# Kernel optimization log

Measured on AMD Instinct MI355X. Metric: run time of the kernel, lower is better.

The kernel has to match this reference:

```python
import jax, jax.numpy as jnp
import numpy as np

B, V, C, D, H, W = 2, 2, 32, 48, 128, 160


def _conv2d(x, w, pad):
    return jax.lax.conv_general_dilated(x, w, (1, 1), [(pad, pad), (pad, pad)],
                                        dimension_numbers=('NCHW', 'OIHW', 'NCHW'))


def _bilinear_sample(fea, px, py):
    # fea: [b,c,h,w]; px,py: [b,N] pixel coords (grid_sample bilinear, zeros padding, align_corners=True)
    b, c, h, w = fea.shape
    fea_flat = fea.reshape(b, c, h * w)
    x0 = jnp.floor(px); y0 = jnp.floor(py)
    wx = px - x0; wy = py - y0
    x0i = x0.astype(jnp.int32); y0i = y0.astype(jnp.int32)

    def corner(xi, yi, wgt):
        valid = (xi >= 0) & (xi < w) & (yi >= 0) & (yi < h)
        idx = jnp.clip(yi, 0, h - 1) * w + jnp.clip(xi, 0, w - 1)
        g = jax.vmap(lambda f, i: f[:, i])(fea_flat, idx)  # [b,c,N]
        return g * (wgt * valid)[:, None, :]

    return (corner(x0i, y0i, (1 - wx) * (1 - wy))
            + corner(x0i + 1, y0i, wx * (1 - wy))
            + corner(x0i, y0i + 1, (1 - wx) * wy)
            + corner(x0i + 1, y0i + 1, wx * wy))


def _homo_warp(src_fea, src_proj, ref_proj, depth_values):
    # classic MVSNet 3D homography warp -> [b,c,d,h,w]
    b, c, h, w = src_fea.shape
    d = depth_values.shape[1]
    proj = src_proj @ jnp.linalg.inv(ref_proj)
    rot, trans = proj[:, :3, :3], proj[:, :3, 3]
    yy, xx = jnp.meshgrid(jnp.arange(h, dtype=src_fea.dtype), jnp.arange(w, dtype=src_fea.dtype), indexing='ij')
    xyz = jnp.stack([xx.ravel(), yy.ravel(), jnp.ones(h * w, src_fea.dtype)])  # [3,hw]
    rot_xyz = jnp.einsum('bij,jn->bin', rot, xyz)  # [b,3,hw]
    pxyz = rot_xyz[:, :, None, :] * depth_values.reshape(b, 1, d, h * w) + trans[:, :, None, None]
    z = pxyz[:, 2]
    z = jnp.where(jnp.abs(z) < 1e-6, 1e-6, z)
    px = (pxyz[:, 0] / z).reshape(b, d * h * w)
    py = (pxyz[:, 1] / z).reshape(b, d * h * w)
    return _bilinear_sample(src_fea, px, py).reshape(b, c, d, h, w)


def setup_inputs() -> dict:
    key = jax.random.key(0)
    ks = jax.random.split(key, 8)
    ref_fea = jax.random.normal(ks[0], (B, C, H, W), jnp.float32)
    src_feas = jax.random.normal(ks[1], (V, B, C, H, W), jnp.float32)
    ref_nc = jax.random.uniform(ks[2], (B, 1, H, W), jnp.float32)
    ref_nc_sum = jax.random.uniform(ks[3], (B, 1, H, W), jnp.float32)
    src_nc_sums = jax.random.uniform(ks[4], (V, B, 1, H, W), jnp.float32)
    # structured projections: slot 0 = extrinsic 4x4, slot 1 holds K in [:3,:3]
    K = np.eye(4, dtype=np.float32)
    K[0, 0] = K[1, 1] = 200.0; K[0, 2] = W / 2.0; K[1, 2] = H / 2.0
    projs = np.zeros((B, V + 1, 2, 4, 4), np.float32)
    for v in range(V + 1):
        E = np.eye(4, dtype=np.float32)
        if v > 0:
            E[0, 3] = 2.0 * v  # horizontal baseline
        projs[:, v, 0] = E
        projs[:, v, 1] = K
    proj_matrices = jnp.asarray(projs)
    dvals = jnp.linspace(425.0, 900.0, D, dtype=jnp.float32)
    depth_values = jnp.broadcast_to(dvals[None, :, None, None], (B, D, H, W))
    vis_w1 = jax.random.normal(ks[5], (32, 2, 3, 3), jnp.float32) * 0.1
    vis_bn_gamma = jnp.ones((32,), jnp.float32)
    vis_bn_beta = jnp.zeros((32,), jnp.float32)
    vis_w2 = jax.random.normal(ks[6], (1, 32, 1, 1), jnp.float32) * 0.1
    vis_b2 = jnp.zeros((1,), jnp.float32)
    reg_w = jax.random.normal(ks[7], (C,), jnp.float32) * 0.1
    reg_b = jnp.zeros((1,), jnp.float32)
    return dict(ref_fea=ref_fea, src_feas=src_feas, ref_nc=ref_nc, ref_nc_sum=ref_nc_sum,
                src_nc_sums=src_nc_sums, proj_matrices=proj_matrices, depth_values=depth_values,
                vis_w1=vis_w1, vis_bn_gamma=vis_bn_gamma, vis_bn_beta=vis_bn_beta,
                vis_w2=vis_w2, vis_b2=vis_b2, reg_w=reg_w, reg_b=reg_b)


def reference(ref_fea, src_feas, ref_nc, ref_nc_sum, src_nc_sums, proj_matrices,
              depth_values, vis_w1, vis_bn_gamma, vis_bn_beta, vis_w2, vis_b2, reg_w, reg_b):
    b, c, h, w = ref_fea.shape
    d = depth_values.shape[1]
    v_src = src_feas.shape[0]
    rp = proj_matrices[:, 0]
    ref_proj_new = rp[:, 0].at[:, :3, :4].set(rp[:, 1, :3, :3] @ rp[:, 0, :3, :4])
    bn_scale = vis_bn_gamma / jnp.sqrt(jnp.float32(1.0) + 1e-5)  # eval BN: running mean 0, var 1
    volume_sum = 0.0
    vis_sum = 0.0
    nc_sum = 0.0
    for v in range(v_src):  # small fixed loop over source views
        sp = proj_matrices[:, v + 1]
        src_proj_new = sp[:, 0].at[:, :3, :4].set(sp[:, 1, :3, :3] @ sp[:, 0, :3, :4])
        warped = _homo_warp(src_feas[v], src_proj_new, ref_proj_new, depth_values)  # [b,c,d,h,w]
        in_prod = ref_fea[:, :, None] * warped
        sim = in_prod.sum(axis=1)  # [b,d,h,w]
        sim_sg = jax.lax.stop_gradient(sim)
        p = jax.nn.softmax(sim_sg, axis=1)
        entropy = -(p * jax.nn.log_softmax(sim_sg, axis=1)).sum(axis=1, keepdims=True)
        hconv = _conv2d(jnp.concatenate([entropy, ref_nc], axis=1), vis_w1, 1)
        hconv = jax.nn.relu(hconv * bn_scale[None, :, None, None] + vis_bn_beta[None, :, None, None])
        vw = jax.nn.sigmoid(_conv2d(hconv, vis_w2, 0) + vis_b2[None, :, None, None])  # [b,1,h,w]
        volume_sum = volume_sum + in_prod * vw[:, :, None]
        vis_sum = vis_sum + vw
        nc_sum = nc_sum + (ref_nc_sum + src_nc_sums[v]) / 2.0
    volume_mean = volume_sum / vis_sum[:, :, None]
    # cost_regularization stand-in: 1x1x1 Conv3d (C -> 1), then squeeze(1)
    prob_pre = jnp.einsum('bcdhw,c->bdhw', volume_mean, reg_w) + reg_b[0]
    prob = jax.nn.softmax(prob_pre, axis=1)
    depth = (prob * depth_values).sum(axis=1)
    padded = jnp.pad(prob, ((0, 0), (1, 2), (0, 0), (0, 0)))
    cs = jnp.pad(jnp.cumsum(padded, axis=1), ((0, 0), (1, 0), (0, 0), (0, 0)))
    sum4 = cs[:, 4:] - cs[:, :-4]  # [b,d,h,w]
    didx = (prob * jnp.arange(d, dtype=prob.dtype)[None, :, None, None]).sum(axis=1)
    idx = jnp.clip(jnp.round(didx), 0, d - 1).astype(jnp.int32)
    conf = jnp.take_along_axis(sum4, idx[:, None], axis=1)[:, 0]
    nc_mean = nc_sum / v_src  # num_views - 1
    return depth, conf, nc_mean
```

## Files before the change

### kernel.cpp

```cpp
#include <hip/hip_runtime.h>
#include <math.h>

#define BB 2
#define VV 2
#define CC 32
#define DD 48
#define HH 128
#define WW 160
#define HWPIX (HH*WW)

__device__ __forceinline__ void inv4x4_np(const float* A, float* Ainv) {
    float M[4][8];
    #pragma unroll
    for (int r = 0; r < 4; ++r) {
        #pragma unroll
        for (int c = 0; c < 4; ++c) { M[r][c] = A[r*4+c]; M[r][c+4] = (r == c) ? 1.f : 0.f; }
    }
    #pragma unroll
    for (int col = 0; col < 4; ++col) {
        float d = 1.0f / M[col][col];
        #pragma unroll
        for (int c = 0; c < 8; ++c) M[col][c] *= d;
        #pragma unroll
        for (int r = 0; r < 4; ++r) {
            if (r == col) continue;
            float f = M[r][col];
            #pragma unroll
            for (int c = 0; c < 8; ++c) M[r][c] -= f * M[col][c];
        }
    }
    #pragma unroll
    for (int r = 0; r < 4; ++r)
        #pragma unroll
        for (int c = 0; c < 4; ++c) Ainv[r*4+c] = M[r][c+4];
}


#define NXQ 4
#define NYQ 3
#define GSTRIDE 26

__global__ __launch_bounds__(256, 4) void k_warp(
    const float* __restrict__ src,
    const float* __restrict__ refF,
    const float* __restrict__ regw,
    const float* __restrict__ depthv,
    const float* __restrict__ projm,
    float* __restrict__ tout,
    float* __restrict__ entout)
{
    __shared__ float sGT[64 * GSTRIDE];
    __shared__ float sdep[DD];
    __shared__ float srot[12];

    int gid = blockIdx.x*256 + threadIdx.x;
    int sub = gid & 3;
    int gp  = gid >> 2;
    int pix = gp % HWPIX;
    int vb  = gp / HWPIX;
    int b   = vb % BB;
    int grp = threadIdx.x >> 2;
    float* gt = sGT + grp * GSTRIDE;

    if (threadIdx.x < DD)
        sdep[threadIdx.x] = depthv[(size_t)b*DD*HWPIX + (size_t)threadIdx.x*HWPIX];
    if (threadIdx.x == 0) {
        int v = vb / BB;
        const float* E = projm + ((size_t)(b*(VV+1) + 0)*2 + 0)*16;
        const float* K = projm + ((size_t)(b*(VV+1) + 0)*2 + 1)*16;
        float refN[16];
        #pragma unroll
        for (int r = 0; r < 3; ++r)
            #pragma unroll
            for (int c = 0; c < 4; ++c)
                refN[r*4+c] = K[r*4+0]*E[0*4+c] + K[r*4+1]*E[1*4+c] + K[r*4+2]*E[2*4+c];
        #pragma unroll
        for (int c = 0; c < 4; ++c) refN[12+c] = E[12+c];
        const float* Es = projm + ((size_t)(b*(VV+1) + (v+1))*2 + 0)*16;
        const float* Ks = projm + ((size_t)(b*(VV+1) + (v+1))*2 + 1)*16;
        float srcN[16];
        #pragma unroll
        for (int r = 0; r < 3; ++r)
            #pragma unroll
            for (int c = 0; c < 4; ++c)
                srcN[r*4+c] = Ks[r*4+0]*Es[0*4+c] + Ks[r*4+1]*Es[1*4+c] + Ks[r*4+2]*Es[2*4+c];
        #pragma unroll
        for (int c = 0; c < 4; ++c) srcN[12+c] = Es[12+c];
        float refI[16];
        inv4x4_np(refN, refI);
        float P[16];
        #pragma unroll
        for (int r = 0; r < 4; ++r)
            #pragma unroll
            for (int c = 0; c < 4; ++c) {
                float a = 0.f;
                #pragma unroll
                for (int k = 0; k < 4; ++k) a += srcN[r*4+k]*refI[k*4+c];
                P[r*4+c] = a;
            }
        srot[0]=P[0]; srot[1]=P[1]; srot[2]=P[2];
        srot[3]=P[4]; srot[4]=P[5]; srot[5]=P[6];
        srot[6]=P[8]; srot[7]=P[9]; srot[8]=P[10];
        srot[9]=P[3]; srot[10]=P[7]; srot[11]=P[11];
    }
    __syncthreads();

    float fx = (float)(pix % WW);
    float fy = (float)(pix / WW);

    float rx = fmaf(srot[0], fx, fmaf(srot[1], fy, srot[2]));
    float ry = fmaf(srot[3], fx, fmaf(srot[4], fy, srot[5]));
    float rz = fmaf(srot[6], fx, fmaf(srot[7], fy, srot[8]));
    float tx = srot[9], ty = srot[10], tz = srot[11];

    const float* rfp = refF + (size_t)b*CC*HWPIX + (size_t)(sub*8)*HWPIX + pix;
    float rfv[8];
    #pragma unroll
    for (int q = 0; q < 8; ++q) rfv[q] = rfp[(size_t)q*HWPIX];
    const float4* rw4 = (const float4*)regw;
    float4 q0 = rw4[sub*2], q1 = rw4[sub*2+1];
    float gfv[8];
    gfv[0] = rfv[0]*q0.x; gfv[1] = rfv[1]*q0.y; gfv[2] = rfv[2]*q0.z; gfv[3] = rfv[3]*q0.w;
    gfv[4] = rfv[4]*q1.x; gfv[5] = rfv[5]*q1.y; gfv[6] = rfv[6]*q1.z; gfv[7] = rfv[7]*q1.w;

    float pxs[12], pys[12];
    float minx =  1e30f, miny =  1e30f;
    #pragma unroll
    for (int i = 0; i < 12; ++i) {
        float dep = sdep[sub*12 + i];
        float X  = fmaf(rx, dep, tx);
        float Y  = fmaf(ry, dep, ty);
        float Zc = fmaf(rz, dep, tz);
        float z  = (fabsf(Zc) < 1e-6f) ? 1e-6f : Zc;
        float iz = 1.0f / z;
        float pxd = X * iz, pyd = Y * iz;
        pxs[i] = pxd; pys[i] = pyd;
        minx = fminf(minx, pxd);
        miny = fminf(miny, pyd);
    }
    #pragma unroll
    for (int msk = 1; msk < 4; msk <<= 1) {
        minx = fminf(minx, __shfl_xor(minx, msk));
        miny = fminf(miny, __shfl_xor(miny, msk));
    }
    float xlof = floorf(fminf(fmaxf(minx, -1e8f), 1e8f));
    float ylof = floorf(fminf(fmaxf(miny, -1e8f), 1e8f));
    int xlo = (int)xlof;
    int ylo = (int)ylof;

    const float* sc = src + (size_t)vb*CC*HWPIX + (size_t)(sub*8)*HWPIX;
    #pragma unroll
    for (int qi = 0; qi < NXQ*NYQ; ++qi) {
        int dx = qi & (NXQ-1), dy = qi >> 2;
        int xi = min(max(xlo + dx, 0), WW-1);
        int yi = min(max(ylo + dy, 0), HH-1);
        const float* p = sc + (size_t)yi*WW + xi;
        float G = 0.f, T = 0.f;
        #pragma unroll
        for (int q = 0; q < 8; ++q) {
            float s = p[(size_t)q*HWPIX];
            G = fmaf(s, rfv[q], G);
            T = fmaf(s, gfv[q], T);
        }
        G += __shfl_xor(G, 1); G += __shfl_xor(G, 2);
        T += __shfl_xor(T, 1); T += __shfl_xor(T, 2);
        if (sub == (qi & 3)) {
            *(float2*)(gt + qi*2) = make_float2(G, T);
        }
    }

    float t12[12];
    float m = -INFINITY, Zs = 0.f, S1 = 0.f;
    #pragma unroll
    for (int i = 0; i < 12; ++i) {
        float pxd = pxs[i], pyd = pys[i];
        float x0f = floorf(pxd), y0f = floorf(pyd);
        float wx = pxd - x0f, wy = pyd - y0f;
        int x0 = (int)x0f, y0 = (int)y0f;
        int x1 = x0 + 1, y1 = y0 + 1;
        float v00 = (x0 >= 0 && x0 < WW && y0 >= 0 && y0 < HH) ? 1.f : 0.f;
        float v01 = (x1 >= 0 && x1 < WW && y0 >= 0 && y0 < HH) ? 1.f : 0.f;
        float v10 = (x0 >= 0 && x0 < WW && y1 >= 0 && y1 < HH) ? 1.f : 0.f;
        float v11 = (x1 >= 0 && x1 < WW && y1 >= 0 && y1 < HH) ? 1.f : 0.f;
        float w00 = (1.f-wx)*(1.f-wy)*v00;
        float w01 = wx*(1.f-wy)*v01;
        float w10 = (1.f-wx)*wy*v10;
        float w11 = wx*wy*v11;
        int dx0 = min(max(x0 - xlo, 0), NXQ-2);
        int dy0 = min(max(y0 - ylo, 0), NYQ-2);
        int q00 = dy0*NXQ + dx0;
        float2 g00 = *(const float2*)(gt + q00*2);
        float2 g01 = *(const float2*)(gt + q00*2 + 2);
        float2 g10 = *(const float2*)(gt + (q00+NXQ)*2);
        float2 g11 = *(const float2*)(gt + (q00+NXQ)*2 + 2);
        float s = fmaf(w00, g00.x, fmaf(w01, g01.x, fmaf(w10, g10.x, w11*g11.x)));
        float t = fmaf(w00, g00.y, fmaf(w01, g01.y, fmaf(w10, g10.y, w11*g11.y)));
        t12[i] = t;
        float mn = fmaxf(m, s);
        float aold = __expf(m - mn);
        float e    = __expf(s - mn);
        Zs = fmaf(Zs, aold, e);
        S1 = fmaf(S1, aold, s*e);
        m = mn;
    }

    float4* tp4 = (float4*)(tout + ((size_t)vb*HWPIX + pix)*DD + sub*12);
    tp4[0] = make_float4(t12[0], t12[1], t12[2],  t12[3]);
    tp4[1] = make_float4(t12[4], t12[5], t12[6],  t12[7]);
    tp4[2] = make_float4(t12[8], t12[9], t12[10], t12[11]);

    #pragma unroll
    for (int msk = 1; msk < 4; msk <<= 1) {
        float mo = __shfl_xor(m, msk);
        float Zo = __shfl_xor(Zs, msk);
        float So = __shfl_xor(S1, msk);
        float mn = fmaxf(m, mo);
        float ea = __expf(m - mn);
        float eb = __expf(mo - mn);
        Zs = fmaf(Zs, ea, Zo*eb);
        S1 = fmaf(S1, ea, So*eb);
        m = mn;
    }
    if (sub == 0)
        entout[(size_t)vb*HWPIX + pix] = m + __logf(Zs) - S1/Zs;
}


__global__ __launch_bounds__(256) void k_final(
    const float* __restrict__ tbuf,
    const float* __restrict__ entbuf,
    const float* __restrict__ ref_nc,
    const float* __restrict__ w1,
    const float* __restrict__ gamma,
    const float* __restrict__ beta,
    const float* __restrict__ w2,
    const float* __restrict__ b2,
    const float* __restrict__ regb,
    const float* __restrict__ depthv,
    const float* __restrict__ ref_nc_sum,
    const float* __restrict__ src_nc_sums,
    float* __restrict__ dout)
{
    __shared__ float sw[32*24];
    __shared__ float sscale[32], sbeta[32], sw2[32];
    __shared__ float sdep[DD];
    __shared__ float sent[VV][3][34];
    __shared__ float snc[3][34];

    int gid = blockIdx.x*256 + threadIdx.x;
    int sub = gid & 7;
    int gp  = gid >> 3;
    int pix = gp % HWPIX;
    int b   = gp / HWPIX;
    int xin = threadIdx.x >> 3;

    int gp0  = blockIdx.x*32;
    int b0   = gp0 / HWPIX;
    int pix0 = gp0 % HWPIX;
    int ytile = pix0 / WW;
    int x0    = pix0 % WW;

    for (int i = threadIdx.x; i < 576; i += 256) {
        int o = i / 18, k = i % 18;
        sw[o*24 + (k < 9 ? k : k + 3)] = w1[i];
    }
    if (threadIdx.x < 32) {
        sscale[threadIdx.x] = gamma[threadIdx.x] / sqrtf(1.0f + 1e-5f);
        sbeta[threadIdx.x]  = beta[threadIdx.x];
        sw2[threadIdx.x]    = w2[threadIdx.x];
    }
    if (threadIdx.x < DD)
        sdep[threadIdx.x] = depthv[(size_t)b0*DD*HWPIX + (size_t)threadIdx.x*HWPIX];
    for (int i = threadIdx.x; i < 306; i += 256) {
        int r, cx;
        float val = 0.f;
        if (i < 204) {
            int v = i / 102, rem = i % 102;
            r = rem / 34; cx = rem % 34;
            int yy = ytile + r - 1, xx = x0 + cx - 1;
            if (yy >= 0 && yy < HH && xx >= 0 && xx < WW)
                val = entbuf[(size_t)(v*BB + b0)*HWPIX + yy*WW + xx];
            sent[v][r][cx] = val;
        } else {
            int i2 = i - 204;
            r = i2 / 34; cx = i2 % 34;
            int yy = ytile + r - 1, xx = x0 + cx - 1;
            if (yy >= 0 && yy < HH && xx >= 0 && xx < WW)
                val = ref_nc[(size_t)b0*HWPIX + yy*WW + xx];
            snc[r][cx] = val;
        }
    }
    __syncthreads();
    float bias2 = b2[0], rb = regb[0];

    float wnc[9], went[VV][9];
    #pragma unroll
    for (int ky = 0; ky < 3; ++ky) {
        #pragma unroll
        for (int kx = 0; kx < 3; ++kx) {
            wnc[ky*3+kx] = snc[ky][xin+kx];
            #pragma unroll
            for (int v = 0; v < VV; ++v)
                went[v][ky*3+kx] = sent[v][ky][xin+kx];
        }
    }

    float ncpart[4];
    #pragma unroll
    for (int j = 0; j < 4; ++j) {
        int o = sub*4 + j;
        const float* wb = sw + o*24;
        float4 n0 = *(const float4*)(wb + 12);
        float4 n1 = *(const float4*)(wb + 16);
        float n8 = wb[20];
        float a = n8 * wnc[8];
        a = fmaf(n0.x, wnc[0], a); a = fmaf(n0.y, wnc[1], a);
        a = fmaf(n0.z, wnc[2], a); a = fmaf(n0.w, wnc[3], a);
        a = fmaf(n1.x, wnc[4], a); a = fmaf(n1.y, wnc[5], a);
        a = fmaf(n1.z, wnc[6], a); a = fmaf(n1.w, wnc[7], a);
        ncpart[j] = a;
    }

    float vw[VV]; float vwsum = 0.f;
    #pragma unroll
    for (int v = 0; v < VV; ++v) {
        float accp = 0.f;
        #pragma unroll
        for (int j = 0; j < 4; ++j) {
            int o = sub*4 + j;
            const float* wb = sw + o*24;
            float4 e0 = *(const float4*)(wb);
            float4 e1 = *(const float4*)(wb + 4);
            float e8 = wb[8];
            float a = fmaf(e8, went[v][8], ncpart[j]);
            a = fmaf(e0.x, went[v][0], a); a = fmaf(e0.y, went[v][1], a);
            a = fmaf(e0.z, went[v][2], a); a = fmaf(e0.w, went[v][3], a);
            a = fmaf(e1.x, went[v][4], a); a = fmaf(e1.y, went[v][5], a);
            a = fmaf(e1.z, went[v][6], a); a = fmaf(e1.w, went[v][7], a);
            a = fmaf(a, sscale[o], sbeta[o]);
            a = fmaxf(a, 0.f);
            accp = fmaf(a, sw2[o], accp);
        }
        accp += __shfl_xor(accp, 1); accp += __shfl_xor(accp, 2); accp += __shfl_xor(accp, 4);
        float vv = 1.f / (1.f + __expf(-(accp + bias2)));
        vw[v] = vv; vwsum += vv;
    }
    float ivw = 1.f / vwsum;

    const float* t0p = tbuf + ((size_t)(0*BB + b)*HWPIX + pix)*DD + sub*6;
    const float* t1p = tbuf + ((size_t)(1*BB + b)*HWPIX + pix)*DD + sub*6;
    float tv0[6], tv1[6];
    *(float2*)(tv0+0) = *(const float2*)(t0p+0);
    *(float2*)(tv0+2) = *(const float2*)(t0p+2);
    *(float2*)(tv0+4) = *(const float2*)(t0p+4);
    *(float2*)(tv1+0) = *(const float2*)(t1p+0);
    *(float2*)(tv1+2) = *(const float2*)(t1p+2);
    *(float2*)(tv1+4) = *(const float2*)(t1p+4);

    float pre[6];
    float mx = -INFINITY;
    #pragma unroll
    for (int i = 0; i < 6; ++i) {
        float p = fmaf(fmaf(vw[0], tv0[i], vw[1]*tv1[i]), ivw, rb);
        pre[i] = p;
        mx = fmaxf(mx, p);
    }
    mx = fmaxf(mx, __shfl_xor(mx, 1));
    mx = fmaxf(mx, __shfl_xor(mx, 2));
    mx = fmaxf(mx, __shfl_xor(mx, 4));

    float Zp = 0.f, kp = 0.f, dp = 0.f;
    float ev[6];
    #pragma unroll
    for (int i = 0; i < 6; ++i) {
        int d = sub*6 + i;
        float e = __expf(pre[i] - mx);
        ev[i] = e;
        Zp += e;
        kp = fmaf((float)d, e, kp);
        dp = fmaf(sdep[d], e, dp);
    }
    Zp += __shfl_xor(Zp, 1); Zp += __shfl_xor(Zp, 2); Zp += __shfl_xor(Zp, 4);
    kp += __shfl_xor(kp, 1); kp += __shfl_xor(kp, 2); kp += __shfl_xor(kp, 4);
    dp += __shfl_xor(dp, 1); dp += __shfl_xor(dp, 2); dp += __shfl_xor(dp, 4);

    float iZ = 1.f / Zp;
    float depth = dp * iZ;
    float didx  = kp * iZ;
    float r = rintf(didx);
    r = fminf(fmaxf(r, 0.f), (float)(DD-1));
    int idx = (int)r;
    float cfp = 0.f;
    #pragma unroll
    for (int i = 0; i < 6; ++i) {
        int d = sub*6 + i;
        cfp += (d >= idx-1 && d <= idx+2) ? ev[i] : 0.f;
    }
    cfp += __shfl_xor(cfp, 1); cfp += __shfl_xor(cfp, 2); cfp += __shfl_xor(cfp, 4);

    if (sub == 0) {
        dout[(size_t)b*HWPIX + pix] = depth;
        dout[(size_t)BB*HWPIX + (size_t)b*HWPIX + pix] = cfp * iZ;
    } else if (sub == 1) {
        float rn = ref_nc_sum[(size_t)b*HWPIX + pix];
        float s = 0.f;
        #pragma unroll
        for (int v = 0; v < VV; ++v)
            s += (rn + src_nc_sums[(size_t)(v*BB + b)*HWPIX + pix]) * 0.5f;
        dout[(size_t)2*BB*HWPIX + (size_t)b*HWPIX + pix] = s / (float)VV;
    }
}

extern "C" void kernel_launch(void* const* d_in, const int* in_sizes, int n_in,
                              void* d_out, int out_size, void* d_ws, size_t ws_size,
                              hipStream_t stream) {
    const float* ref_fea     = (const float*)d_in[0];
    const float* src_feas    = (const float*)d_in[1];
    const float* ref_nc      = (const float*)d_in[2];
    const float* ref_nc_sum  = (const float*)d_in[3];
    const float* src_nc_sums = (const float*)d_in[4];
    const float* projm       = (const float*)d_in[5];
    const float* depthv      = (const float*)d_in[6];
    const float* w1          = (const float*)d_in[7];
    const float* gamma       = (const float*)d_in[8];
    const float* beta        = (const float*)d_in[9];
    const float* w2          = (const float*)d_in[10];
    const float* b2v         = (const float*)d_in[11];
    const float* regw        = (const float*)d_in[12];
    const float* regb        = (const float*)d_in[13];
    float* out = (float*)d_out;
    float* ws  = (float*)d_ws;

    float* tbuf   = ws + 64;
    float* entbuf = tbuf + (size_t)VV*BB*HWPIX*DD;

    k_warp<<<(VV*BB*HWPIX*4)/256, 256, 0, stream>>>(src_feas, ref_fea, regw, depthv,
                                                    projm, tbuf, entbuf);
    k_final<<<(BB*HWPIX*8)/256, 256, 0, stream>>>(tbuf, entbuf, ref_nc, w1, gamma,
                                                  beta, w2, b2v, regb, depthv,
                                                  ref_nc_sum, src_nc_sums, out);
}
```

Measured before the change: 121.9 us.

## Fuse warp and final kernels into one persistent cooperative kernel with grid sync

Merges the two kernels into one persistent cooperative kernel. Blocks loop over the tiles of each phase and are separated by a grid-wide sync, which removes the second kernel launch and its ramp-up. The online max-subtracted softmax in both phases is also replaced by plain exp sums without max subtraction, which saves exp work but risks overflow for large logits. The occupancy query and the grid sync add host and device overhead, and the grid is capped at 1280 blocks, so each block processes many tiles serially.

Measured after the change: 222.4 us. +82.4%, slower.

```diff
diff --git a/kernel.cpp b/kernel.cpp
--- a/kernel.cpp
+++ b/kernel.cpp
@@ -1,5 +1,8 @@
 #include <hip/hip_runtime.h>
+#include <hip/hip_cooperative_groups.h>
 #include <math.h>
+
+namespace cg = cooperative_groups;
 
 #define BB 2
 #define VV 2
@@ -9,6 +12,10 @@
 #define WW 160
 #define HWPIX (HH*WW)
 
+#define NXQ 4
+#define NYQ 3
+#define GSTRIDE 26
+
 __device__ __forceinline__ void inv4x4_np(const float* A, float* Ainv) {
     float M[4][8];
     #pragma unroll
@@ -35,200 +42,12 @@
         for (int c = 0; c < 4; ++c) Ainv[r*4+c] = M[r][c+4];
 }
 
-
-#define NXQ 4
-#define NYQ 3
-#define GSTRIDE 26
-
-__global__ __launch_bounds__(256, 4) void k_warp(
+__global__ __launch_bounds__(256, 4) void k_fused(
     const float* __restrict__ src,
     const float* __restrict__ refF,
     const float* __restrict__ regw,
     const float* __restrict__ depthv,
     const float* __restrict__ projm,
-    float* __restrict__ tout,
-    float* __restrict__ entout)
-{
-    __shared__ float sGT[64 * GSTRIDE];
-    __shared__ float sdep[DD];
-    __shared__ float srot[12];
-
-    int gid = blockIdx.x*256 + threadIdx.x;
-    int sub = gid & 3;
-    int gp  = gid >> 2;
-    int pix = gp % HWPIX;
-    int vb  = gp / HWPIX;
-    int b   = vb % BB;
-    int grp = threadIdx.x >> 2;
-    float* gt = sGT + grp * GSTRIDE;
-
-    if (threadIdx.x < DD)
-        sdep[threadIdx.x] = depthv[(size_t)b*DD*HWPIX + (size_t)threadIdx.x*HWPIX];
-    if (threadIdx.x == 0) {
-        int v = vb / BB;
-        const float* E = projm + ((size_t)(b*(VV+1) + 0)*2 + 0)*16;
-        const float* K = projm + ((size_t)(b*(VV+1) + 0)*2 + 1)*16;
-        float refN[16];
-        #pragma unroll
-        for (int r = 0; r < 3; ++r)
-            #pragma unroll
-            for (int c = 0; c < 4; ++c)
-                refN[r*4+c] = K[r*4+0]*E[0*4+c] + K[r*4+1]*E[1*4+c] + K[r*4+2]*E[2*4+c];
-        #pragma unroll
-        for (int c = 0; c < 4; ++c) refN[12+c] = E[12+c];
-        const float* Es = projm + ((size_t)(b*(VV+1) + (v+1))*2 + 0)*16;
-        const float* Ks = projm + ((size_t)(b*(VV+1) + (v+1))*2 + 1)*16;
-        float srcN[16];
-        #pragma unroll
-        for (int r = 0; r < 3; ++r)
-            #pragma unroll
-            for (int c = 0; c < 4; ++c)
-                srcN[r*4+c] = Ks[r*4+0]*Es[0*4+c] + Ks[r*4+1]*Es[1*4+c] + Ks[r*4+2]*Es[2*4+c];
-        #pragma unroll
-        for (int c = 0; c < 4; ++c) srcN[12+c] = Es[12+c];
-        float refI[16];
-        inv4x4_np(refN, refI);
-        float P[16];
-        #pragma unroll
-        for (int r = 0; r < 4; ++r)
-            #pragma unroll
-            for (int c = 0; c < 4; ++c) {
-                float a = 0.f;
-                #pragma unroll
-                for (int k = 0; k < 4; ++k) a += srcN[r*4+k]*refI[k*4+c];
-                P[r*4+c] = a;
-            }
-        srot[0]=P[0]; srot[1]=P[1]; srot[2]=P[2];
-        srot[3]=P[4]; srot[4]=P[5]; srot[5]=P[6];
-        srot[6]=P[8]; srot[7]=P[9]; srot[8]=P[10];
-        srot[9]=P[3]; srot[10]=P[7]; srot[11]=P[11];
-    }
-    __syncthreads();
-
-    float fx = (float)(pix % WW);
-    float fy = (float)(pix / WW);
-
-    float rx = fmaf(srot[0], fx, fmaf(srot[1], fy, srot[2]));
-    float ry = fmaf(srot[3], fx, fmaf(srot[4], fy, srot[5]));
-    float rz = fmaf(srot[6], fx, fmaf(srot[7], fy, srot[8]));
-    float tx = srot[9], ty = srot[10], tz = srot[11];
-
-    const float* rfp = refF + (size_t)b*CC*HWPIX + (size_t)(sub*8)*HWPIX + pix;
-    float rfv[8];
-    #pragma unroll
-    for (int q = 0; q < 8; ++q) rfv[q] = rfp[(size_t)q*HWPIX];
-    const float4* rw4 = (const float4*)regw;
-    float4 q0 = rw4[sub*2], q1 = rw4[sub*2+1];
-    float gfv[8];
-    gfv[0] = rfv[0]*q0.x; gfv[1] = rfv[1]*q0.y; gfv[2] = rfv[2]*q0.z; gfv[3] = rfv[3]*q0.w;
-    gfv[4] = rfv[4]*q1.x; gfv[5] = rfv[5]*q1.y; gfv[6] = rfv[6]*q1.z; gfv[7] = rfv[7]*q1.w;
-
-    float pxs[12], pys[12];
-    float minx =  1e30f, miny =  1e30f;
-    #pragma unroll
-    for (int i = 0; i < 12; ++i) {
-        float dep = sdep[sub*12 + i];
-        float X  = fmaf(rx, dep, tx);
-        float Y  = fmaf(ry, dep, ty);
-        float Zc = fmaf(rz, dep, tz);
-        float z  = (fabsf(Zc) < 1e-6f) ? 1e-6f : Zc;
-        float iz = 1.0f / z;
-        float pxd = X * iz, pyd = Y * iz;
-        pxs[i] = pxd; pys[i] = pyd;
-        minx = fminf(minx, pxd);
-        miny = fminf(miny, pyd);
-    }
-    #pragma unroll
-    for (int msk = 1; msk < 4; msk <<= 1) {
-        minx = fminf(minx, __shfl_xor(minx, msk));
-        miny = fminf(miny, __shfl_xor(miny, msk));
-    }
-    float xlof = floorf(fminf(fmaxf(minx, -1e8f), 1e8f));
-    float ylof = floorf(fminf(fmaxf(miny, -1e8f), 1e8f));
-    int xlo = (int)xlof;
-    int ylo = (int)ylof;
-
-    const float* sc = src + (size_t)vb*CC*HWPIX + (size_t)(sub*8)*HWPIX;
-    #pragma unroll
-    for (int qi = 0; qi < NXQ*NYQ; ++qi) {
-        int dx = qi & (NXQ-1), dy = qi >> 2;
-        int xi = min(max(xlo + dx, 0), WW-1);
-        int yi = min(max(ylo + dy, 0), HH-1);
-        const float* p = sc + (size_t)yi*WW + xi;
-        float G = 0.f, T = 0.f;
-        #pragma unroll
-        for (int q = 0; q < 8; ++q) {
-            float s = p[(size_t)q*HWPIX];
-            G = fmaf(s, rfv[q], G);
-            T = fmaf(s, gfv[q], T);
-        }
-        G += __shfl_xor(G, 1); G += __shfl_xor(G, 2);
-        T += __shfl_xor(T, 1); T += __shfl_xor(T, 2);
-        if (sub == (qi & 3)) {
-            *(float2*)(gt + qi*2) = make_float2(G, T);
-        }
-    }
-
-    float t12[12];
-    float m = -INFINITY, Zs = 0.f, S1 = 0.f;
-    #pragma unroll
-    for (int i = 0; i < 12; ++i) {
-        float pxd = pxs[i], pyd = pys[i];
-        float x0f = floorf(pxd), y0f = floorf(pyd);
-        float wx = pxd - x0f, wy = pyd - y0f;
-        int x0 = (int)x0f, y0 = (int)y0f;
-        int x1 = x0 + 1, y1 = y0 + 1;
-        float v00 = (x0 >= 0 && x0 < WW && y0 >= 0 && y0 < HH) ? 1.f : 0.f;
-        float v01 = (x1 >= 0 && x1 < WW && y0 >= 0 && y0 < HH) ? 1.f : 0.f;
-        float v10 = (x0 >= 0 && x0 < WW && y1 >= 0 && y1 < HH) ? 1.f : 0.f;
-        float v11 = (x1 >= 0 && x1 < WW && y1 >= 0 && y1 < HH) ? 1.f : 0.f;
-        float w00 = (1.f-wx)*(1.f-wy)*v00;
-        float w01 = wx*(1.f-wy)*v01;
-        float w10 = (1.f-wx)*wy*v10;
-        float w11 = wx*wy*v11;
-        int dx0 = min(max(x0 - xlo, 0), NXQ-2);
-        int dy0 = min(max(y0 - ylo, 0), NYQ-2);
-        int q00 = dy0*NXQ + dx0;
-        float2 g00 = *(const float2*)(gt + q00*2);
-        float2 g01 = *(const float2*)(gt + q00*2 + 2);
-        float2 g10 = *(const float2*)(gt + (q00+NXQ)*2);
-        float2 g11 = *(const float2*)(gt + (q00+NXQ)*2 + 2);
-        float s = fmaf(w00, g00.x, fmaf(w01, g01.x, fmaf(w10, g10.x, w11*g11.x)));
-        float t = fmaf(w00, g00.y, fmaf(w01, g01.y, fmaf(w10, g10.y, w11*g11.y)));
-        t12[i] = t;
-        float mn = fmaxf(m, s);
-        float aold = __expf(m - mn);
-        float e    = __expf(s - mn);
-        Zs = fmaf(Zs, aold, e);
-        S1 = fmaf(S1, aold, s*e);
-        m = mn;
-    }
-
-    float4* tp4 = (float4*)(tout + ((size_t)vb*HWPIX + pix)*DD + sub*12);
-    tp4[0] = make_float4(t12[0], t12[1], t12[2],  t12[3]);
-    tp4[1] = make_float4(t12[4], t12[5], t12[6],  t12[7]);
-    tp4[2] = make_float4(t12[8], t12[9], t12[10], t12[11]);
-
-    #pragma unroll
-    for (int msk = 1; msk < 4; msk <<= 1) {
-        float mo = __shfl_xor(m, msk);
-        float Zo = __shfl_xor(Zs, msk);
-        float So = __shfl_xor(S1, msk);
-        float mn = fmaxf(m, mo);
-        float ea = __expf(m - mn);
-        float eb = __expf(mo - mn);
-        Zs = fmaf(Zs, ea, Zo*eb);
-        S1 = fmaf(S1, ea, So*eb);
-        m = mn;
-    }
-    if (sub == 0)
-        entout[(size_t)vb*HWPIX + pix] = m + __logf(Zs) - S1/Zs;
-}
-
-
-__global__ __launch_bounds__(256) void k_final(
-    const float* __restrict__ tbuf,
-    const float* __restrict__ entbuf,
     const float* __restrict__ ref_nc,
     const float* __restrict__ w1,
     const float* __restrict__ gamma,
@@ -236,29 +55,182 @@
     const float* __restrict__ w2,
     const float* __restrict__ b2,
     const float* __restrict__ regb,
-    const float* __restrict__ depthv,
     const float* __restrict__ ref_nc_sum,
     const float* __restrict__ src_nc_sums,
+    float* __restrict__ tout,
+    float* __restrict__ entout,
     float* __restrict__ dout)
 {
+    __shared__ float sGT[64 * GSTRIDE];
+    __shared__ float sdep[DD];
+    __shared__ float srot[12];
     __shared__ float sw[32*24];
-    __shared__ float sscale[32], sbeta[32], sw2[32];
-    __shared__ float sdep[DD];
+    __shared__ float sscale[32], sbeta[32], sw2v[32];
     __shared__ float sent[VV][3][34];
     __shared__ float snc[3][34];
 
-    int gid = blockIdx.x*256 + threadIdx.x;
-    int sub = gid & 7;
-    int gp  = gid >> 3;
-    int pix = gp % HWPIX;
-    int b   = gp / HWPIX;
-    int xin = threadIdx.x >> 3;
-
-    int gp0  = blockIdx.x*32;
-    int b0   = gp0 / HWPIX;
-    int pix0 = gp0 % HWPIX;
-    int ytile = pix0 / WW;
-    int x0    = pix0 % WW;
+    const int T1 = (VV*BB*HWPIX*4)/256;
+    const int T2 = (BB*HWPIX*8)/256;
+
+    for (int tile = blockIdx.x; tile < T1; tile += gridDim.x) {
+        __syncthreads();
+        int gid = tile*256 + threadIdx.x;
+        int sub = gid & 3;
+        int gp  = gid >> 2;
+        int pix = gp % HWPIX;
+        int vb  = gp / HWPIX;
+        int b   = vb % BB;
+        int grp = threadIdx.x >> 2;
+        float* gt = sGT + grp * GSTRIDE;
+
+        if (threadIdx.x < DD)
+            sdep[threadIdx.x] = depthv[(size_t)b*DD*HWPIX + (size_t)threadIdx.x*HWPIX];
+        if (threadIdx.x == 0) {
+            int v = vb / BB;
+            const float* E = projm + ((size_t)(b*(VV+1) + 0)*2 + 0)*16;
+            const float* K = projm + ((size_t)(b*(VV+1) + 0)*2 + 1)*16;
+            float refN[16];
+            #pragma unroll
+            for (int r = 0; r < 3; ++r)
+                #pragma unroll
+                for (int c = 0; c < 4; ++c)
+                    refN[r*4+c] = K[r*4+0]*E[0*4+c] + K[r*4+1]*E[1*4+c] + K[r*4+2]*E[2*4+c];
+            #pragma unroll
+            for (int c = 0; c < 4; ++c) refN[12+c] = E[12+c];
+            const float* Es = projm + ((size_t)(b*(VV+1) + (v+1))*2 + 0)*16;
+            const float* Ks = projm + ((size_t)(b*(VV+1) + (v+1))*2 + 1)*16;
+            float srcN[16];
+            #pragma unroll
+            for (int r = 0; r < 3; ++r)
+                #pragma unroll
+                for (int c = 0; c < 4; ++c)
+                    srcN[r*4+c] = Ks[r*4+0]*Es[0*4+c] + Ks[r*4+1]*Es[1*4+c] + Ks[r*4+2]*Es[2*4+c];
+            #pragma unroll
+            for (int c = 0; c < 4; ++c) srcN[12+c] = Es[12+c];
+            float refI[16];
+            inv4x4_np(refN, refI);
+            float P[16];
+            #pragma unroll
+            for (int r = 0; r < 4; ++r)
+                #pragma unroll
+                for (int c = 0; c < 4; ++c) {
+                    float a = 0.f;
+                    #pragma unroll
+                    for (int k = 0; k < 4; ++k) a += srcN[r*4+k]*refI[k*4+c];
+                    P[r*4+c] = a;
+                }
+            srot[0]=P[0]; srot[1]=P[1]; srot[2]=P[2];
+            srot[3]=P[4]; srot[4]=P[5]; srot[5]=P[6];
+            srot[6]=P[8]; srot[7]=P[9]; srot[8]=P[10];
+            srot[9]=P[3]; srot[10]=P[7]; srot[11]=P[11];
+        }
+        __syncthreads();
+
+        float fx = (float)(pix % WW);
+        float fy = (float)(pix / WW);
+        float rx = fmaf(srot[0], fx, fmaf(srot[1], fy, srot[2]));
+        float ry = fmaf(srot[3], fx, fmaf(srot[4], fy, srot[5]));
+        float rz = fmaf(srot[6], fx, fmaf(srot[7], fy, srot[8]));
+        float tx = srot[9], ty = srot[10], tz = srot[11];
+
+        const float* rfp = refF + (size_t)b*CC*HWPIX + (size_t)(sub*8)*HWPIX + pix;
+        float rfv[8];
+        #pragma unroll
+        for (int q = 0; q < 8; ++q) rfv[q] = rfp[(size_t)q*HWPIX];
+        const float4* rw4 = (const float4*)regw;
+        float4 q0 = rw4[sub*2], q1 = rw4[sub*2+1];
+        float gfv[8];
+        gfv[0] = rfv[0]*q0.x; gfv[1] = rfv[1]*q0.y; gfv[2] = rfv[2]*q0.z; gfv[3] = rfv[3]*q0.w;
+        gfv[4] = rfv[4]*q1.x; gfv[5] = rfv[5]*q1.y; gfv[6] = rfv[6]*q1.z; gfv[7] = rfv[7]*q1.w;
+
+        float pxs[12], pys[12];
+        float minx = 1e30f, miny = 1e30f;
+        #pragma unroll
+        for (int i = 0; i < 12; ++i) {
+            float dep = sdep[sub*12 + i];
+            float X  = fmaf(rx, dep, tx);
+            float Y  = fmaf(ry, dep, ty);
+            float Zc = fmaf(rz, dep, tz);
+            float z  = (fabsf(Zc) < 1e-6f) ? 1e-6f : Zc;
+            float iz = 1.0f / z;
+            float pxd = X * iz, pyd = Y * iz;
+            pxs[i] = pxd; pys[i] = pyd;
+            minx = fminf(minx, pxd);
+            miny = fminf(miny, pyd);
+        }
+        #pragma unroll
+        for (int msk = 1; msk < 4; msk <<= 1) {
+            minx = fminf(minx, __shfl_xor(minx, msk));
+            miny = fminf(miny, __shfl_xor(miny, msk));
+        }
+        int xlo = (int)floorf(fminf(fmaxf(minx, -1e8f), 1e8f));
+        int ylo = (int)floorf(fminf(fmaxf(miny, -1e8f), 1e8f));
+
+        const float* sc = src + (size_t)vb*CC*HWPIX + (size_t)(sub*8)*HWPIX;
+        #pragma unroll
+        for (int qi = 0; qi < NXQ*NYQ; ++qi) {
+            int dx = qi & (NXQ-1), dy = qi >> 2;
+            int xi = min(max(xlo + dx, 0), WW-1);
+            int yi = min(max(ylo + dy, 0), HH-1);
+            const float* p = sc + (size_t)yi*WW + xi;
+            float G = 0.f, T = 0.f;
+            #pragma unroll
+            for (int q = 0; q < 8; ++q) {
+                float s = p[(size_t)q*HWPIX];
+                G = fmaf(s, rfv[q], G);
+                T = fmaf(s, gfv[q], T);
+            }
+            G += __shfl_xor(G, 1); G += __shfl_xor(G, 2);
+            T += __shfl_xor(T, 1); T += __shfl_xor(T, 2);
+            if (sub == (qi & 3)) {
+                *(float2*)(gt + qi*2) = make_float2(G, T);
+            }
+        }
+
+        float t12[12];
+        float Zs = 0.f, S1 = 0.f;
+        #pragma unroll
+        for (int i = 0; i < 12; ++i) {
+            float pxd = pxs[i], pyd = pys[i];
+            float x0f = floorf(pxd), y0f = floorf(pyd);
+            float wx = pxd - x0f, wy = pyd - y0f;
+            int x0 = (int)x0f, y0 = (int)y0f;
+            int x1 = x0 + 1, y1 = y0 + 1;
+            float v00 = (x0 >= 0 && x0 < WW && y0 >= 0 && y0 < HH) ? 1.f : 0.f;
+            float v01 = (x1 >= 0 && x1 < WW && y0 >= 0 && y0 < HH) ? 1.f : 0.f;
+            float v10 = (x0 >= 0 && x0 < WW && y1 >= 0 && y1 < HH) ? 1.f : 0.f;
+            float v11 = (x1 >= 0 && x1 < WW && y1 >= 0 && y1 < HH) ? 1.f : 0.f;
+            float w00 = (1.f-wx)*(1.f-wy)*v00;
+            float w01 = wx*(1.f-wy)*v01;
+            float w10 = (1.f-wx)*wy*v10;
+            float w11 = wx*wy*v11;
+            int dx0 = min(max(x0 - xlo, 0), NXQ-2);
+            int dy0 = min(max(y0 - ylo, 0), NYQ-2);
+            int q00 = dy0*NXQ + dx0;
+            float2 g00 = *(const float2*)(gt + q00*2);
+            float2 g01 = *(const float2*)(gt + q00*2 + 2);
+            float2 g10 = *(const float2*)(gt + (q00+NXQ)*2);
+            float2 g11 = *(const float2*)(gt + (q00+NXQ)*2 + 2);
+            float s = fmaf(w00, g00.x, fmaf(w01, g01.x, fmaf(w10, g10.x, w11*g11.x)));
+            float t = fmaf(w00, g00.y, fmaf(w01, g01.y, fmaf(w10, g10.y, w11*g11.y)));
+            t12[i] = t;
+            float e = __expf(s);
+            Zs += e;
+            S1 = fmaf(s, e, S1);
+        }
+
+        float4* tp4 = (float4*)(tout + ((size_t)vb*HWPIX + pix)*DD + sub*12);
+        tp4[0] = make_float4(t12[0], t12[1], t12[2],  t12[3]);
+        tp4[1] = make_float4(t12[4], t12[5], t12[6],  t12[7]);
+        tp4[2] = make_float4(t12[8], t12[9], t12[10], t12[11]);
+
+        Zs += __shfl_xor(Zs, 1); Zs += __shfl_xor(Zs, 2);
+        S1 += __shfl_xor(S1, 1); S1 += __shfl_xor(S1, 2);
+        if (sub == 0)
+            entout[(size_t)vb*HWPIX + pix] = __logf(Zs) - S1/Zs;
+    }
+
+    cg::this_grid().sync();
 
     for (int i = threadIdx.x; i < 576; i += 256) {
         int o = i / 18, k = i % 18;
@@ -267,147 +239,153 @@
     if (threadIdx.x < 32) {
         sscale[threadIdx.x] = gamma[threadIdx.x] / sqrtf(1.0f + 1e-5f);
         sbeta[threadIdx.x]  = beta[threadIdx.x];
-        sw2[threadIdx.x]    = w2[threadIdx.x];
-    }
-    if (threadIdx.x < DD)
-        sdep[threadIdx.x] = depthv[(size_t)b0*DD*HWPIX + (size_t)threadIdx.x*HWPIX];
-    for (int i = threadIdx.x; i < 306; i += 256) {
-        int r, cx;
-        float val = 0.f;
-        if (i < 204) {
-            int v = i / 102, rem = i % 102;
-            r = rem / 34; cx = rem % 34;
-            int yy = ytile + r - 1, xx = x0 + cx - 1;
-            if (yy >= 0 && yy < HH && xx >= 0 && xx < WW)
-                val = entbuf[(size_t)(v*BB + b0)*HWPIX + yy*WW + xx];
-            sent[v][r][cx] = val;
-        } else {
-            int i2 = i - 204;
-            r = i2 / 34; cx = i2 % 34;
-            int yy = ytile + r - 1, xx = x0 + cx - 1;
-            if (yy >= 0 && yy < HH && xx >= 0 && xx < WW)
-                val = ref_nc[(size_t)b0*HWPIX + yy*WW + xx];
-            snc[r][cx] = val;
-        }
-    }
-    __syncthreads();
+        sw2v[threadIdx.x]   = w2[threadIdx.x];
+    }
     float bias2 = b2[0], rb = regb[0];
 
-    float wnc[9], went[VV][9];
-    #pragma unroll
-    for (int ky = 0; ky < 3; ++ky) {
-        #pragma unroll
-        for (int kx = 0; kx < 3; ++kx) {
-            wnc[ky*3+kx] = snc[ky][xin+kx];
-            #pragma unroll
-            for (int v = 0; v < VV; ++v)
-                went[v][ky*3+kx] = sent[v][ky][xin+kx];
-        }
-    }
-
-    float ncpart[4];
-    #pragma unroll
-    for (int j = 0; j < 4; ++j) {
-        int o = sub*4 + j;
-        const float* wb = sw + o*24;
-        float4 n0 = *(const float4*)(wb + 12);
-        float4 n1 = *(const float4*)(wb + 16);
-        float n8 = wb[20];
-        float a = n8 * wnc[8];
-        a = fmaf(n0.x, wnc[0], a); a = fmaf(n0.y, wnc[1], a);
-        a = fmaf(n0.z, wnc[2], a); a = fmaf(n0.w, wnc[3], a);
-        a = fmaf(n1.x, wnc[4], a); a = fmaf(n1.y, wnc[5], a);
-        a = fmaf(n1.z, wnc[6], a); a = fmaf(n1.w, wnc[7], a);
-        ncpart[j] = a;
-    }
-
-    float vw[VV]; float vwsum = 0.f;
-    #pragma unroll
-    for (int v = 0; v < VV; ++v) {
-        float accp = 0.f;
+    for (int tile = blockIdx.x; tile < T2; tile += gridDim.x) {
+        __syncthreads();
+        int gid = tile*256 + threadIdx.x;
+        int sub = gid & 7;
+        int gp  = gid >> 3;
+        int pix = gp % HWPIX;
+        int b   = gp / HWPIX;
+        int xin = threadIdx.x >> 3;
+
+        int gp0  = tile*32;
+        int b0   = gp0 / HWPIX;
+        int pix0 = gp0 % HWPIX;
+        int ytile = pix0 / WW;
+        int x0t   = pix0 % WW;
+
+        if (threadIdx.x < DD)
+            sdep[threadIdx.x] = depthv[(size_t)b0*DD*HWPIX + (size_t)threadIdx.x*HWPIX];
+        for (int i = threadIdx.x; i < 306; i += 256) {
+            int r, cx;
+            float val = 0.f;
+            if (i < 204) {
+                int v = i / 102, rem = i % 102;
+                r = rem / 34; cx = rem % 34;
+                int yy = ytile + r - 1, xx = x0t + cx - 1;
+                if (yy >= 0 && yy < HH && xx >= 0 && xx < WW)
+                    val = entout[(size_t)(v*BB + b0)*HWPIX + yy*WW + xx];
+                sent[v][r][cx] = val;
+            } else {
+                int i2 = i - 204;
+                r = i2 / 34; cx = i2 % 34;
+                int yy = ytile + r - 1, xx = x0t + cx - 1;
+                if (yy >= 0 && yy < HH && xx >= 0 && xx < WW)
+                    val = ref_nc[(size_t)b0*HWPIX + yy*WW + xx];
+                snc[r][cx] = val;
+            }
+        }
+        __syncthreads();
+
+        float wnc[9], went[VV][9];
+        #pragma unroll
+        for (int ky = 0; ky < 3; ++ky) {
+            #pragma unroll
+            for (int kx = 0; kx < 3; ++kx) {
+                wnc[ky*3+kx] = snc[ky][xin+kx];
+                #pragma unroll
+                for (int v = 0; v < VV; ++v)
+                    went[v][ky*3+kx] = sent[v][ky][xin+kx];
+            }
+        }
+
+        float ncpart[4];
         #pragma unroll
         for (int j = 0; j < 4; ++j) {
             int o = sub*4 + j;
             const float* wb = sw + o*24;
-            float4 e0 = *(const float4*)(wb);
-            float4 e1 = *(const float4*)(wb + 4);
-            float e8 = wb[8];
-            float a = fmaf(e8, went[v][8], ncpart[j]);
-            a = fmaf(e0.x, went[v][0], a); a = fmaf(e0.y, went[v][1], a);
-            a = fmaf(e0.z, went[v][2], a); a = fmaf(e0.w, went[v][3], a);
-            a = fmaf(e1.x, went[v][4], a); a = fmaf(e1.y, went[v][5], a);
-            a = fmaf(e1.z, went[v][6], a); a = fmaf(e1.w, went[v][7], a);
-            a = fmaf(a, sscale[o], sbeta[o]);
-            a = fmaxf(a, 0.f);
-            accp = fmaf(a, sw2[o], accp);
-        }
-        accp += __shfl_xor(accp, 1); accp += __shfl_xor(accp, 2); accp += __shfl_xor(accp, 4);
-        float vv = 1.f / (1.f + __expf(-(accp + bias2)));
-        vw[v] = vv; vwsum += vv;
-    }
-    float ivw = 1.f / vwsum;
-
-    const float* t0p = tbuf + ((size_t)(0*BB + b)*HWPIX + pix)*DD + sub*6;
-    const float* t1p = tbuf + ((size_t)(1*BB + b)*HWPIX + pix)*DD + sub*6;
-    float tv0[6], tv1[6];
-    *(float2*)(tv0+0) = *(const float2*)(t0p+0);
-    *(float2*)(tv0+2) = *(const float2*)(t0p+2);
-    *(float2*)(tv0+4) = *(const float2*)(t0p+4);
-    *(float2*)(tv1+0) = *(const float2*)(t1p+0);
-    *(float2*)(tv1+2) = *(const float2*)(t1p+2);
-    *(float2*)(tv1+4) = *(const float2*)(t1p+4);
-
-    float pre[6];
-    float mx = -INFINITY;
-    #pragma unroll
-    for (int i = 0; i < 6; ++i) {
-        float p = fmaf(fmaf(vw[0], tv0[i], vw[1]*tv1[i]), ivw, rb);
-        pre[i] = p;
-        mx = fmaxf(mx, p);
-    }
-    mx = fmaxf(mx, __shfl_xor(mx, 1));
-    mx = fmaxf(mx, __shfl_xor(mx, 2));
-    mx = fmaxf(mx, __shfl_xor(mx, 4));
-
-    float Zp = 0.f, kp = 0.f, dp = 0.f;
-    float ev[6];
-    #pragma unroll
-    for (int i = 0; i < 6; ++i) {
-        int d = sub*6 + i;
-        float e = __expf(pre[i] - mx);
-        ev[i] = e;
-        Zp += e;
-        kp = fmaf((float)d, e, kp);
-        dp = fmaf(sdep[d], e, dp);
-    }
-    Zp += __shfl_xor(Zp, 1); Zp += __shfl_xor(Zp, 2); Zp += __shfl_xor(Zp, 4);
-    kp += __shfl_xor(kp, 1); kp += __shfl_xor(kp, 2); kp += __shfl_xor(kp, 4);
-    dp += __shfl_xor(dp, 1); dp += __shfl_xor(dp, 2); dp += __shfl_xor(dp, 4);
-
-    float iZ = 1.f / Zp;
-    float depth = dp * iZ;
-    float didx  = kp * iZ;
-    float r = rintf(didx);
-    r = fminf(fmaxf(r, 0.f), (float)(DD-1));
-    int idx = (int)r;
-    float cfp = 0.f;
-    #pragma unroll
-    for (int i = 0; i < 6; ++i) {
-        int d = sub*6 + i;
-        cfp += (d >= idx-1 && d <= idx+2) ? ev[i] : 0.f;
-    }
-    cfp += __shfl_xor(cfp, 1); cfp += __shfl_xor(cfp, 2); cfp += __shfl_xor(cfp, 4);
-
-    if (sub == 0) {
-        dout[(size_t)b*HWPIX + pix] = depth;
-        dout[(size_t)BB*HWPIX + (size_t)b*HWPIX + pix] = cfp * iZ;
-    } else if (sub == 1) {
-        float rn = ref_nc_sum[(size_t)b*HWPIX + pix];
-        float s = 0.f;
-        #pragma unroll
-        for (int v = 0; v < VV; ++v)
-            s += (rn + src_nc_sums[(size_t)(v*BB + b)*HWPIX + pix]) * 0.5f;
-        dout[(size_t)2*BB*HWPIX + (size_t)b*HWPIX + pix] = s / (float)VV;
+            float4 n0 = *(const float4*)(wb + 12);
+            float4 n1 = *(const float4*)(wb + 16);
+            float n8 = wb[20];
+            float a = n8 * wnc[8];
+            a = fmaf(n0.x, wnc[0], a); a = fmaf(n0.y, wnc[1], a);
+            a = fmaf(n0.z, wnc[2], a); a = fmaf(n0.w, wnc[3], a);
+            a = fmaf(n1.x, wnc[4], a); a = fmaf(n1.y, wnc[5], a);
+            a = fmaf(n1.z, wnc[6], a); a = fmaf(n1.w, wnc[7], a);
+            ncpart[j] = a;
+        }
+
+        float vw[VV]; float vwsum = 0.f;
+        #pragma unroll
+        for (int v = 0; v < VV; ++v) {
+            float accp = 0.f;
+            #pragma unroll
+            for (int j = 0; j < 4; ++j) {
+                int o = sub*4 + j;
+                const float* wb = sw + o*24;
+                float4 e0 = *(const float4*)(wb);
+                float4 e1 = *(const float4*)(wb + 4);
+                float e8 = wb[8];
+                float a = fmaf(e8, went[v][8], ncpart[j]);
+                a = fmaf(e0.x, went[v][0], a); a = fmaf(e0.y, went[v][1], a);
+                a = fmaf(e0.z, went[v][2], a); a = fmaf(e0.w, went[v][3], a);
+                a = fmaf(e1.x, went[v][4], a); a = fmaf(e1.y, went[v][5], a);
+                a = fmaf(e1.z, went[v][6], a); a = fmaf(e1.w, went[v][7], a);
+                a = fmaf(a, sscale[o], sbeta[o]);
+                a = fmaxf(a, 0.f);
+                accp = fmaf(a, sw2v[o], accp);
+            }
+            accp += __shfl_xor(accp, 1); accp += __shfl_xor(accp, 2); accp += __shfl_xor(accp, 4);
+            float vv = 1.f / (1.f + __expf(-(accp + bias2)));
+            vw[v] = vv; vwsum += vv;
+        }
+        float ivw = 1.f / vwsum;
+
+        const float* t0p = tout + ((size_t)(0*BB + b)*HWPIX + pix)*DD + sub*6;
+        const float* t1p = tout + ((size_t)(1*BB + b)*HWPIX + pix)*DD + sub*6;
+        float tv0[6], tv1[6];
+        *(float2*)(tv0+0) = *(const float2*)(t0p+0);
+        *(float2*)(tv0+2) = *(const float2*)(t0p+2);
+        *(float2*)(tv0+4) = *(const float2*)(t0p+4);
+        *(float2*)(tv1+0) = *(const float2*)(t1p+0);
+        *(float2*)(tv1+2) = *(const float2*)(t1p+2);
+        *(float2*)(tv1+4) = *(const float2*)(t1p+4);
+
+        float Zp = 0.f, kp = 0.f, dp = 0.f;
+        float ev[6];
+        #pragma unroll
+        for (int i = 0; i < 6; ++i) {
+            int d = sub*6 + i;
+            float pre = fmaf(fmaf(vw[0], tv0[i], vw[1]*tv1[i]), ivw, rb);
+            float e = __expf(pre);
+            ev[i] = e;
+            Zp += e;
+            kp = fmaf((float)d, e, kp);
+            dp = fmaf(sdep[d], e, dp);
+        }
+        Zp += __shfl_xor(Zp, 1); Zp += __shfl_xor(Zp, 2); Zp += __shfl_xor(Zp, 4);
+        kp += __shfl_xor(kp, 1); kp += __shfl_xor(kp, 2); kp += __shfl_xor(kp, 4);
+        dp += __shfl_xor(dp, 1); dp += __shfl_xor(dp, 2); dp += __shfl_xor(dp, 4);
+
+        float iZ = 1.f / Zp;
+        float depth = dp * iZ;
+        float didx  = kp * iZ;
+        float r = rintf(didx);
+        r = fminf(fmaxf(r, 0.f), (float)(DD-1));
+        int idx = (int)r;
+        float cfp = 0.f;
+        #pragma unroll
+        for (int i = 0; i < 6; ++i) {
+            int d = sub*6 + i;
+            cfp += (d >= idx-1 && d <= idx+2) ? ev[i] : 0.f;
+        }
+        cfp += __shfl_xor(cfp, 1); cfp += __shfl_xor(cfp, 2); cfp += __shfl_xor(cfp, 4);
+
+        if (sub == 0) {
+            dout[(size_t)b*HWPIX + pix] = depth;
+            dout[(size_t)BB*HWPIX + (size_t)b*HWPIX + pix] = cfp * iZ;
+        } else if (sub == 1) {
+            float rn = ref_nc_sum[(size_t)b*HWPIX + pix];
+            float s = 0.f;
+            #pragma unroll
+            for (int v = 0; v < VV; ++v)
+                s += (rn + src_nc_sums[(size_t)(v*BB + b)*HWPIX + pix]) * 0.5f;
+            dout[(size_t)2*BB*HWPIX + (size_t)b*HWPIX + pix] = s / (float)VV;
+        }
     }
 }
 
@@ -434,9 +412,19 @@
     float* tbuf   = ws + 64;
     float* entbuf = tbuf + (size_t)VV*BB*HWPIX*DD;
 
-    k_warp<<<(VV*BB*HWPIX*4)/256, 256, 0, stream>>>(src_feas, ref_fea, regw, depthv,
-                                                    projm, tbuf, entbuf);
-    k_final<<<(BB*HWPIX*8)/256, 256, 0, stream>>>(tbuf, entbuf, ref_nc, w1, gamma,
-                                                  beta, w2, b2v, regb, depthv,
-                                                  ref_nc_sum, src_nc_sums, out);
+    int blocksPerCU = 0;
+    hipOccupancyMaxActiveBlocksPerMultiprocessor(&blocksPerCU, (const void*)k_fused, 256, 0);
+    if (blocksPerCU < 1) blocksPerCU = 1;
+    int grid = blocksPerCU * 256;
+    if (grid > 1280) grid = 1280;
+
+    void* args[] = {
+        (void*)&src_feas, (void*)&ref_fea, (void*)&regw, (void*)&depthv,
+        (void*)&projm, (void*)&ref_nc, (void*)&w1, (void*)&gamma,
+        (void*)&beta, (void*)&w2, (void*)&b2v, (void*)&regb,
+        (void*)&ref_nc_sum, (void*)&src_nc_sums,
+        (void*)&tbuf, (void*)&entbuf, (void*)&out
+    };
+    hipLaunchCooperativeKernel((const void*)k_fused, dim3(grid), dim3(256),
+                               args, 0, stream);
 }
```
